# Kernel optimization log

Hardware: AMD Instinct MI355X
Metric: run time of the kernel (lower is better)

Reference implementation:

```python
import jax, jax.numpy as jnp
import numpy as np

EPS = 1e-5

def _bn(z, gamma, beta):
    mu = z.mean(axis=0)
    var = z.var(axis=0)  # biased, matches torch BN normalization
    return (z - mu) * jax.lax.rsqrt(var + EPS) * gamma + beta

def _sage_bn_relu(h, src, dst, n_nodes, Wl, bl, Wr, gamma, beta):
    # SAGEConv (mean aggr): out = lin_l(mean_{j in N(i)} h_j) + lin_r(h_i)
    msg = h[src]                                               # [E, d] gather
    agg = jax.ops.segment_sum(msg, dst, num_segments=n_nodes)  # [N, d]
    cnt = jax.ops.segment_sum(jnp.ones((src.shape[0], 1), h.dtype), dst,
                              num_segments=n_nodes)            # [N, 1]
    agg = jnp.where(cnt > 0, agg / jnp.maximum(cnt, 1.0), 0.0)
    out = agg @ Wl.T + bl + h @ Wr.T
    return jax.nn.relu(_bn(out, gamma, beta))

def setup_inputs() -> dict:
    key = jax.random.key(0)
    N, E, d, out_c, L, U = 50000, 800000, 128, 128, 3, 256
    ks = jax.random.split(key, 16)
    s = 1.0 / np.sqrt(d)
    return {
        "x": jax.random.normal(ks[0], (N, d), jnp.float32),
        "edge_index": jax.random.randint(ks[1], (2, E), 0, N, jnp.int64),
        "atom_mask": jax.random.uniform(ks[2], (N, 1), jnp.float32),
        "u_index": jax.random.randint(ks[3], (U,), 0, N, jnp.int64),
        "lin_l_w": jax.random.uniform(ks[4], (L, d, d), jnp.float32, -s, s),
        "lin_l_b": jax.random.uniform(ks[5], (L, d), jnp.float32, -s, s),
        "lin_r_w": jax.random.uniform(ks[6], (L, d, d), jnp.float32, -s, s),
        "bn_gamma": jnp.ones((L, d), jnp.float32),
        "bn_beta": jnp.zeros((L, d), jnp.float32),
        "ro_w1": jax.random.uniform(ks[7], (d, d), jnp.float32, -s, s),
        "ro_b1": jax.random.uniform(ks[8], (d,), jnp.float32, -s, s),
        "ro_bn_gamma": jnp.ones((d,), jnp.float32),
        "ro_bn_beta": jnp.zeros((d,), jnp.float32),
        "ro_w2": jax.random.uniform(ks[9], (out_c, d), jnp.float32, -s, s),
        "ro_b2": jax.random.uniform(ks[10], (out_c,), jnp.float32, -s, s),
    }

def reference(x, edge_index, atom_mask, u_index, lin_l_w, lin_l_b, lin_r_w,
              bn_gamma, bn_beta, ro_w1, ro_b1, ro_bn_gamma, ro_bn_beta,
              ro_w2, ro_b2):
    N = x.shape[0]
    src, dst = edge_index[0], edge_index[1]
    h = x
    for l in range(lin_l_w.shape[0]):
        h = _sage_bn_relu(h, src, dst, N, lin_l_w[l], lin_l_b[l],
                          lin_r_w[l], bn_gamma[l], bn_beta[l])
    state = h[u_index]                                         # [U, d]
    z = jax.nn.relu(_bn(h @ ro_w1.T + ro_b1, ro_bn_gamma, ro_bn_beta))
    atom = (z @ ro_w2.T + ro_b2) * atom_mask                   # [N, out]
    return (h, atom, state)
```

## Files before the change

kernel.cpp:

```cpp
#include <hip/hip_runtime.h>

#define D 128

typedef __attribute__((ext_vector_type(8))) short bf16x8;
typedef __attribute__((ext_vector_type(4))) float f32x4;

__device__ __forceinline__ ushort f2b(float f) {
  union { float f; unsigned u; } a; a.f = f;
  unsigned u = a.u;
  return (ushort)((u + 0x7fffu + ((u >> 16) & 1u)) >> 16);
}
__device__ __forceinline__ float b2f_lo(unsigned v) {
  union { unsigned u; float f; } a; a.u = v << 16; return a.f;
}
__device__ __forceinline__ float b2f_hi(unsigned v) {
  union { unsigned u; float f; } a; a.u = v & 0xffff0000u; return a.f;
}

__global__ void k_cast_pad(const float* __restrict__ s, ushort* __restrict__ d, int n4, int np4) {
  int i = blockIdx.x * blockDim.x + threadIdx.x;
  if (i >= np4) return;
  uint2 pk;
  if (i < n4) {
    float4 v = *(const float4*)&s[i * 4];
    pk.x = (unsigned)f2b(v.x) | ((unsigned)f2b(v.y) << 16);
    pk.y = (unsigned)f2b(v.z) | ((unsigned)f2b(v.w) << 16);
  } else {
    pk = make_uint2(0u, 0u);
  }
  *(uint2*)&d[i * 4] = pk;
}

__global__ void k_castw(const float* __restrict__ wl, const float* __restrict__ wr,
                        const float* __restrict__ w1, const float* __restrict__ w2,
                        ushort* __restrict__ dst, int LDD) {
  int i = blockIdx.x * blockDim.x + threadIdx.x;
  int total = 2 * LDD + 2 * D * D;
  if (i >= total) return;
  float v;
  if (i < LDD) v = wl[i];
  else if (i < 2 * LDD) v = wr[i - LDD];
  else if (i < 2 * LDD + D * D) v = w1[i - 2 * LDD];
  else v = w2[i - 2 * LDD - D * D];
  dst[i] = f2b(v);
}

__global__ void k_hist(const int* __restrict__ dstI, int* __restrict__ cnt, int E) {
  int e = blockIdx.x * blockDim.x + threadIdx.x;
  if (e < E) atomicAdd(&cnt[dstI[e]], 1);
}
__global__ void k_scan1(const int* __restrict__ cnt, int* __restrict__ off,
                        int* __restrict__ bsum, int n) {
  __shared__ int sd[256];
  int t = threadIdx.x;
  int i = blockIdx.x * 256 + t;
  int x = (i < n) ? cnt[i] : 0;
  sd[t] = x;
  __syncthreads();
  for (int s = 1; s < 256; s <<= 1) {
    int v = (t >= s) ? sd[t - s] : 0;
    __syncthreads();
    sd[t] += v;
    __syncthreads();
  }
  if (i < n) off[i] = sd[t] - x;
  if (t == 255) bsum[blockIdx.x] = sd[255];
}
__global__ void k_scan2(const int* __restrict__ bsum, int* __restrict__ boff, int nb) {
  __shared__ int sd[256];
  int t = threadIdx.x;
  int x = (t < nb) ? bsum[t] : 0;
  sd[t] = x;
  __syncthreads();
  for (int s = 1; s < 256; s <<= 1) {
    int v = (t >= s) ? sd[t - s] : 0;
    __syncthreads();
    sd[t] += v;
    __syncthreads();
  }
  if (t < nb) boff[t] = sd[t] - x;
}
__global__ void k_scan3(int* __restrict__ off, const int* __restrict__ boff,
                        int* __restrict__ cursor, int n) {
  int i = blockIdx.x * blockDim.x + threadIdx.x;
  if (i < n) {
    int v = off[i] + boff[i >> 8];
    off[i] = v;
    cursor[i] = v;
  }
}
__global__ void k_fill(const int* __restrict__ srcI, const int* __restrict__ dstI,
                       int* __restrict__ cursor, int* __restrict__ eidx, int E) {
  int e = blockIdx.x * blockDim.x + threadIdx.x;
  if (e < E) {
    int p = atomicAdd(&cursor[dstI[e]], 1);
    eidx[p] = srcI[e];
  }
}

__global__ void k_agg(const ushort* __restrict__ hb, const int* __restrict__ off,
                      const int* __restrict__ eidx, ushort* __restrict__ aggb,
                      int N, int Np, int E) {
  int g = (int)(blockIdx.x * (blockDim.x >> 4) + (threadIdx.x >> 4));
  int sub = threadIdx.x & 15;
  if (g >= Np) return;
  ushort* dst = &aggb[(size_t)g * D + sub * 8];
  if (g >= N) { *(uint4*)dst = make_uint4(0u, 0u, 0u, 0u); return; }
  int start = off[g];
  int end = (g == N - 1) ? E : off[g + 1];
  float s0 = 0.f, s1 = 0.f, s2 = 0.f, s3 = 0.f, s4 = 0.f, s5 = 0.f, s6 = 0.f, s7 = 0.f;
#pragma unroll 4
  for (int e = start; e < end; ++e) {
    int sn = eidx[e];
    uint4 v = *(const uint4*)&hb[(size_t)sn * D + sub * 8];
    s0 += b2f_lo(v.x); s1 += b2f_hi(v.x);
    s2 += b2f_lo(v.y); s3 += b2f_hi(v.y);
    s4 += b2f_lo(v.z); s5 += b2f_hi(v.z);
    s6 += b2f_lo(v.w); s7 += b2f_hi(v.w);
  }
  float inv = (end > start) ? 1.0f / (float)(end - start) : 0.0f;
  uint4 o;
  o.x = (unsigned)f2b(s0 * inv) | ((unsigned)f2b(s1 * inv) << 16);
  o.y = (unsigned)f2b(s2 * inv) | ((unsigned)f2b(s3 * inv) << 16);
  o.z = (unsigned)f2b(s4 * inv) | ((unsigned)f2b(s5 * inv) << 16);
  o.w = (unsigned)f2b(s6 * inv) | ((unsigned)f2b(s7 * inv) << 16);
  *(uint4*)dst = o;
}

template <bool DUAL, bool MASK, bool STATS, bool OUTBF16>
__global__ __launch_bounds__(256) void k_mm(
    const ushort* __restrict__ A1, const ushort* __restrict__ W1,
    const float* __restrict__ bias,
    const ushort* __restrict__ A2, const ushort* __restrict__ W2,
    const float* __restrict__ mask,
    void* __restrict__ outv, float* __restrict__ sums, int N) {
  __shared__ float ls[2 * D];
  int t = threadIdx.x;
  int lane = t & 63;
  int wid = t >> 6;
  int wr = wid >> 1, wc = wid & 1;
  int r0 = blockIdx.x * 128 + wr * 64;
  int c0 = wc * 64;
  int lr = lane & 15;
  int lk = (lane >> 4) * 8;

  f32x4 acc[4][4];
#pragma unroll
  for (int i = 0; i < 4; ++i)
#pragma unroll
    for (int j = 0; j < 4; ++j) acc[i][j] = (f32x4){0.f, 0.f, 0.f, 0.f};

#pragma unroll
  for (int ks = 0; ks < 4; ++ks) {
    int kb = ks * 32 + lk;
    bf16x8 a1[4], a2[4];
#pragma unroll
    for (int rt = 0; rt < 4; ++rt) {
      a1[rt] = *(const bf16x8*)&A1[(size_t)(r0 + rt * 16 + lr) * D + kb];
      if (DUAL) a2[rt] = *(const bf16x8*)&A2[(size_t)(r0 + rt * 16 + lr) * D + kb];
    }
#pragma unroll
    for (int jt = 0; jt < 4; ++jt) {
      bf16x8 b1 = *(const bf16x8*)&W1[(size_t)(c0 + jt * 16 + lr) * D + kb];
#pragma unroll
      for (int rt = 0; rt < 4; ++rt)
        acc[rt][jt] = __builtin_amdgcn_mfma_f32_16x16x32_bf16(a1[rt], b1, acc[rt][jt], 0, 0, 0);
      if (DUAL) {
        bf16x8 b2 = *(const bf16x8*)&W2[(size_t)(c0 + jt * 16 + lr) * D + kb];
#pragma unroll
        for (int rt = 0; rt < 4; ++rt)
          acc[rt][jt] = __builtin_amdgcn_mfma_f32_16x16x32_bf16(a2[rt], b2, acc[rt][jt], 0, 0, 0);
      }
    }
  }

  if (STATS) {
    if (t < 2 * D) ls[t] = 0.f;
    __syncthreads();
  }

  int crow = (lane >> 4) * 4;
  float s1v[4], s2v[4];
#pragma unroll
  for (int jt = 0; jt < 4; ++jt) { s1v[jt] = 0.f; s2v[jt] = 0.f; }

  float* outf = (float*)outv;
  ushort* outb = (ushort*)outv;
#pragma unroll
  for (int rt = 0; rt < 4; ++rt) {
    int rbase = r0 + rt * 16 + crow;
#pragma unroll
    for (int jt = 0; jt < 4; ++jt) {
      int col = c0 + jt * 16 + lr;
      float bv = bias[col];
#pragma unroll
      for (int rg = 0; rg < 4; ++rg) {
        int row = rbase + rg;
        if (row < N) {
          float v = acc[rt][jt][rg] + bv;
          if (MASK) v *= mask[row];
          if (OUTBF16) outb[(size_t)row * D + col] = f2b(v);
          else outf[(size_t)row * D + col] = v;
          if (STATS) { s1v[jt] += v; s2v[jt] += v * v; }
        }
      }
    }
  }

  if (STATS) {
#pragma unroll
    for (int jt = 0; jt < 4; ++jt) {
      float a = s1v[jt], b = s2v[jt];
      a += __shfl_xor(a, 16, 64); a += __shfl_xor(a, 32, 64);
      b += __shfl_xor(b, 16, 64); b += __shfl_xor(b, 32, 64);
      if (lane < 16) {
        int col = c0 + jt * 16 + lane;
        atomicAdd(&ls[col], a);
        atomicAdd(&ls[D + col], b);
      }
    }
    __syncthreads();
    if (t < 2 * D) atomicAdd(&sums[t], ls[t]);
  }
}

template <bool F32OUT>
__global__ void k_bnrelu(const ushort* __restrict__ pre, const float* __restrict__ sums,
                         const float* __restrict__ gamma, const float* __restrict__ beta,
                         float* __restrict__ fout, ushort* __restrict__ bout,
                         int N, int Np, float invN) {
  int i4 = blockIdx.x * blockDim.x + threadIdx.x;
  if (i4 >= Np * (D / 4)) return;
  int row = i4 >> 5;
  int c4 = (i4 & 31) * 4;
  uint2 pk;
  if (row < N) {
    uint2 pv = *(const uint2*)&pre[(size_t)row * D + c4];
    float4 v = make_float4(b2f_lo(pv.x), b2f_hi(pv.x), b2f_lo(pv.y), b2f_hi(pv.y));
    float4 s = *(const float4*)&sums[c4];
    float4 q = *(const float4*)&sums[D + c4];
    float4 g = *(const float4*)&gamma[c4];
    float4 b = *(const float4*)&beta[c4];
    float mu, var, sc, sh;
    mu = s.x * invN; var = fmaxf(q.x * invN - mu * mu, 0.f);
    sc = g.x * rsqrtf(var + 1e-5f); sh = b.x - mu * sc;
    v.x = fmaxf(fmaf(v.x, sc, sh), 0.f);
    mu = s.y * invN; var = fmaxf(q.y * invN - mu * mu, 0.f);
    sc = g.y * rsqrtf(var + 1e-5f); sh = b.y - mu * sc;
    v.y = fmaxf(fmaf(v.y, sc, sh), 0.f);
    mu = s.z * invN; var = fmaxf(q.z * invN - mu * mu, 0.f);
    sc = g.z * rsqrtf(var + 1e-5f); sh = b.z - mu * sc;
    v.z = fmaxf(fmaf(v.z, sc, sh), 0.f);
    mu = s.w * invN; var = fmaxf(q.w * invN - mu * mu, 0.f);
    sc = g.w * rsqrtf(var + 1e-5f); sh = b.w - mu * sc;
    v.w = fmaxf(fmaf(v.w, sc, sh), 0.f);
    if (F32OUT) *(float4*)&fout[(size_t)row * D + c4] = v;
    pk.x = (unsigned)f2b(v.x) | ((unsigned)f2b(v.y) << 16);
    pk.y = (unsigned)f2b(v.z) | ((unsigned)f2b(v.w) << 16);
  } else {
    pk = make_uint2(0u, 0u);
  }
  *(uint2*)&bout[(size_t)row * D + c4] = pk;
}

__global__ void k_gather(const float* __restrict__ h, const int* __restrict__ uidx,
                         float* __restrict__ outp, int U) {
  int u = blockIdx.x;
  int t = threadIdx.x;
  int s = uidx[u];
  *(float4*)&outp[(size_t)u * D + t * 4] = *(const float4*)&h[(size_t)s * D + t * 4];
}

extern "C" void kernel_launch(void* const* d_in, const int* in_sizes, int n_in,
                              void* d_out, int out_size, void* d_ws, size_t ws_size,
                              hipStream_t stream) {
  const float* x        = (const float*)d_in[0];
  const int*   edge     = (const int*)d_in[1];
  const float* amask    = (const float*)d_in[2];
  const int*   uindex   = (const int*)d_in[3];
  const float* lin_l_w  = (const float*)d_in[4];
  const float* lin_l_b  = (const float*)d_in[5];
  const float* lin_r_w  = (const float*)d_in[6];
  const float* bn_gamma = (const float*)d_in[7];
  const float* bn_beta  = (const float*)d_in[8];
  const float* ro_w1    = (const float*)d_in[9];
  const float* ro_b1    = (const float*)d_in[10];
  const float* ro_bng   = (const float*)d_in[11];
  const float* ro_bnb   = (const float*)d_in[12];
  const float* ro_w2    = (const float*)d_in[13];
  const float* ro_b2    = (const float*)d_in[14];

  const int N = in_sizes[0] / D;
  const int E = in_sizes[1] / 2;
  const int U = in_sizes[3];
  const int L = in_sizes[4] / (D * D);
  const int Np = ((N + 127) / 128) * 128;
  const int LDD = L * D * D;

  const int* srcI = edge;
  const int* dstI = edge + E;

  float* outH     = (float*)d_out;
  float* outAtom  = outH + (size_t)N * D;
  float* outState = outAtom + (size_t)N * D;

  char* w = (char*)d_ws;
  ushort* hb   = (ushort*)w; w += (size_t)Np * D * 2;
  ushort* aggb = (ushort*)w; w += (size_t)Np * D * 2;
  ushort* pre  = (ushort*)w; w += (size_t)Np * D * 2;
  ushort* wall = (ushort*)w; w += (size_t)(2 * LDD + 2 * D * D) * 2;
  float*  sums = (float*)w;  w += 4 * 2 * D * 4;
  int* off    = (int*)w;     w += (size_t)(N + 1) * 4;
  int* cursor = (int*)w;     w += (size_t)N * 4;
  int* bsum   = (int*)w;     w += 1024;
  int* boff   = (int*)w;     w += 1024;
  int* eidx   = (int*)w;     w += (size_t)E * 4;

  ushort* wlb = wall;
  ushort* wrb = wlb + (size_t)LDD;
  ushort* w1b = wrb + (size_t)LDD;
  ushort* w2b = w1b + (size_t)D * D;

  k_cast_pad<<<(Np * D / 4 + 255) / 256, 256, 0, stream>>>(x, hb, N * D / 4, Np * D / 4);
  k_castw<<<(2 * LDD + 2 * D * D + 255) / 256, 256, 0, stream>>>(lin_l_w, lin_r_w, ro_w1, ro_w2, wall, LDD);
  hipMemsetAsync(sums, 0, 4 * 2 * D * 4, stream);

  hipMemsetAsync(cursor, 0, (size_t)N * 4, stream);
  int nbE = (E + 255) / 256;
  int nbN = (N + 255) / 256;
  k_hist<<<nbE, 256, 0, stream>>>(dstI, cursor, E);
  k_scan1<<<nbN, 256, 0, stream>>>(cursor, off, bsum, N);
  k_scan2<<<1, 256, 0, stream>>>(bsum, boff, nbN);
  k_scan3<<<nbN, 256, 0, stream>>>(off, boff, cursor, N);
  k_fill<<<nbE, 256, 0, stream>>>(srcI, dstI, cursor, eidx, E);

  const int mmBlocks = Np / 128;
  const int aggBlocks = Np / 16;
  const int bnBlocks = (Np * (D / 4) + 255) / 256;
  const float invN = 1.0f / (float)N;

  for (int l = 0; l < L; ++l) {
    float* lsums = sums + (size_t)l * 2 * D;
    k_agg<<<aggBlocks, 256, 0, stream>>>(hb, off, eidx, aggb, N, Np, E);
    k_mm<true, false, true, true><<<mmBlocks, 256, 0, stream>>>(
        aggb, wlb + (size_t)l * D * D, lin_l_b + (size_t)l * D,
        hb, wrb + (size_t)l * D * D, nullptr, pre, lsums, N);
    if (l == L - 1)
      k_bnrelu<true><<<bnBlocks, 256, 0, stream>>>(pre, lsums, bn_gamma + (size_t)l * D,
                                                   bn_beta + (size_t)l * D, outH, hb, N, Np, invN);
    else
      k_bnrelu<false><<<bnBlocks, 256, 0, stream>>>(pre, lsums, bn_gamma + (size_t)l * D,
                                                    bn_beta + (size_t)l * D, nullptr, hb, N, Np, invN);
  }

  float* rsums = sums + (size_t)L * 2 * D;
  k_mm<false, false, true, true><<<mmBlocks, 256, 0, stream>>>(
      hb, w1b, ro_b1, nullptr, nullptr, nullptr, pre, rsums, N);
  k_bnrelu<false><<<bnBlocks, 256, 0, stream>>>(pre, rsums, ro_bng, ro_bnb, nullptr, aggb, N, Np, invN);
  k_mm<false, true, false, false><<<mmBlocks, 256, 0, stream>>>(
      aggb, w2b, ro_b2, nullptr, nullptr, amask, outAtom, nullptr, N);
  k_gather<<<U, 32, 0, stream>>>(outH, uindex, outState, U);
}
```

Baseline: 360.3 us.

## Fuse neighbor aggregation into SAGE matmul via LDS and precompute CSR ranks

```diff
diff --git a/kernel.cpp b/kernel.cpp
--- a/kernel.cpp
+++ b/kernel.cpp
@@ -1,6 +1,7 @@
 #include <hip/hip_runtime.h>
 
 #define D 128
+#define LDA 136
 
 typedef __attribute__((ext_vector_type(8))) short bf16x8;
 typedef __attribute__((ext_vector_type(4))) float f32x4;
@@ -45,9 +46,14 @@
   dst[i] = f2b(v);
 }
 
-__global__ void k_hist(const int* __restrict__ dstI, int* __restrict__ cnt, int E) {
+__global__ void k_histrank(const int* __restrict__ dstI, int* __restrict__ cnt,
+                           int* __restrict__ rankdst, int E) {
   int e = blockIdx.x * blockDim.x + threadIdx.x;
-  if (e < E) atomicAdd(&cnt[dstI[e]], 1);
+  if (e < E) {
+    int d = dstI[e];
+    int r = atomicAdd(&cnt[d], 1);
+    rankdst[e] = (r << 16) | d;
+  }
 }
 __global__ void k_scan1(const int* __restrict__ cnt, int* __restrict__ off,
                         int* __restrict__ bsum, int n) {
@@ -80,148 +86,135 @@
   }
   if (t < nb) boff[t] = sd[t] - x;
 }
-__global__ void k_scan3(int* __restrict__ off, const int* __restrict__ boff,
-                        int* __restrict__ cursor, int n) {
+__global__ void k_scan3(int* __restrict__ off, const int* __restrict__ boff, int n) {
   int i = blockIdx.x * blockDim.x + threadIdx.x;
-  if (i < n) {
-    int v = off[i] + boff[i >> 8];
-    off[i] = v;
-    cursor[i] = v;
-  }
-}
-__global__ void k_fill(const int* __restrict__ srcI, const int* __restrict__ dstI,
-                       int* __restrict__ cursor, int* __restrict__ eidx, int E) {
+  if (i < n) off[i] += boff[i >> 8];
+}
+__global__ void k_fill(const int* __restrict__ srcI, const int* __restrict__ rankdst,
+                       const int* __restrict__ off, int* __restrict__ eidx, int E) {
   int e = blockIdx.x * blockDim.x + threadIdx.x;
   if (e < E) {
-    int p = atomicAdd(&cursor[dstI[e]], 1);
-    eidx[p] = srcI[e];
-  }
-}
-
-__global__ void k_agg(const ushort* __restrict__ hb, const int* __restrict__ off,
-                      const int* __restrict__ eidx, ushort* __restrict__ aggb,
-                      int N, int Np, int E) {
-  int g = (int)(blockIdx.x * (blockDim.x >> 4) + (threadIdx.x >> 4));
-  int sub = threadIdx.x & 15;
-  if (g >= Np) return;
-  ushort* dst = &aggb[(size_t)g * D + sub * 8];
-  if (g >= N) { *(uint4*)dst = make_uint4(0u, 0u, 0u, 0u); return; }
-  int start = off[g];
-  int end = (g == N - 1) ? E : off[g + 1];
-  float s0 = 0.f, s1 = 0.f, s2 = 0.f, s3 = 0.f, s4 = 0.f, s5 = 0.f, s6 = 0.f, s7 = 0.f;
-#pragma unroll 4
-  for (int e = start; e < end; ++e) {
-    int sn = eidx[e];
-    uint4 v = *(const uint4*)&hb[(size_t)sn * D + sub * 8];
-    s0 += b2f_lo(v.x); s1 += b2f_hi(v.x);
-    s2 += b2f_lo(v.y); s3 += b2f_hi(v.y);
-    s4 += b2f_lo(v.z); s5 += b2f_hi(v.z);
-    s6 += b2f_lo(v.w); s7 += b2f_hi(v.w);
-  }
-  float inv = (end > start) ? 1.0f / (float)(end - start) : 0.0f;
-  uint4 o;
-  o.x = (unsigned)f2b(s0 * inv) | ((unsigned)f2b(s1 * inv) << 16);
-  o.y = (unsigned)f2b(s2 * inv) | ((unsigned)f2b(s3 * inv) << 16);
-  o.z = (unsigned)f2b(s4 * inv) | ((unsigned)f2b(s5 * inv) << 16);
-  o.w = (unsigned)f2b(s6 * inv) | ((unsigned)f2b(s7 * inv) << 16);
-  *(uint4*)dst = o;
-}
-
-template <bool DUAL, bool MASK, bool STATS, bool OUTBF16>
-__global__ __launch_bounds__(256) void k_mm(
-    const ushort* __restrict__ A1, const ushort* __restrict__ W1,
-    const float* __restrict__ bias,
-    const ushort* __restrict__ A2, const ushort* __restrict__ W2,
-    const float* __restrict__ mask,
-    void* __restrict__ outv, float* __restrict__ sums, int N) {
+    int rd = rankdst[e];
+    int d = rd & 0xFFFF;
+    eidx[off[d] + (rd >> 16)] = srcI[e];
+  }
+}
+
+#define ACC8(V, B)                                        \
+  a[B + 0] += b2f_lo(V.x); a[B + 1] += b2f_hi(V.x);       \
+  a[B + 2] += b2f_lo(V.y); a[B + 3] += b2f_hi(V.y);       \
+  a[B + 4] += b2f_lo(V.z); a[B + 5] += b2f_hi(V.z);       \
+  a[B + 6] += b2f_lo(V.w); a[B + 7] += b2f_hi(V.w);
+
+template <bool AGG>
+__global__ __launch_bounds__(512) void k_fused(
+    const ushort* __restrict__ hin, const ushort* __restrict__ Wl,
+    const ushort* __restrict__ Wr, const float* __restrict__ bias,
+    const int* __restrict__ off, const int* __restrict__ eidx,
+    ushort* __restrict__ pre, float* __restrict__ sums, int N, int E) {
+  __shared__ ushort aggS[128 * LDA];
   __shared__ float ls[2 * D];
   int t = threadIdx.x;
+  int r0 = blockIdx.x * 128;
+
+  if (t < 2 * D) ls[t] = 0.f;
+
+  if (AGG) {
+    int lrow = t >> 2;
+    int row = r0 + lrow;
+    int part = (t & 3) << 5;
+    float a[32];
+#pragma unroll
+    for (int i = 0; i < 32; ++i) a[i] = 0.f;
+    int start = 0, end = 0;
+    if (row < N) { start = off[row]; end = (row == N - 1) ? E : off[row + 1]; }
+    const ushort* hbase = hin + part;
+#pragma unroll 2
+    for (int e = start; e < end; ++e) {
+      int sn = eidx[e];
+      const uint4* p = (const uint4*)(hbase + (size_t)sn * D);
+      uint4 v0 = p[0], v1 = p[1], v2 = p[2], v3 = p[3];
+      ACC8(v0, 0) ACC8(v1, 8) ACC8(v2, 16) ACC8(v3, 24)
+    }
+    float inv = (end > start) ? 1.0f / (float)(end - start) : 0.f;
+    unsigned o[16];
+#pragma unroll
+    for (int i = 0; i < 16; ++i)
+      o[i] = (unsigned)f2b(a[2 * i] * inv) | ((unsigned)f2b(a[2 * i + 1] * inv) << 16);
+    uint4* dst = (uint4*)&aggS[lrow * LDA + part];
+    dst[0] = make_uint4(o[0], o[1], o[2], o[3]);
+    dst[1] = make_uint4(o[4], o[5], o[6], o[7]);
+    dst[2] = make_uint4(o[8], o[9], o[10], o[11]);
+    dst[3] = make_uint4(o[12], o[13], o[14], o[15]);
+  }
+  __syncthreads();
+
   int lane = t & 63;
   int wid = t >> 6;
   int wr = wid >> 1, wc = wid & 1;
-  int r0 = blockIdx.x * 128 + wr * 64;
-  int c0 = wc * 64;
-  int lr = lane & 15;
-  int lk = (lane >> 4) * 8;
-
-  f32x4 acc[4][4];
-#pragma unroll
-  for (int i = 0; i < 4; ++i)
+  int rw = wr * 32, cw = wc * 64;
+  int lr = lane & 15, lk = (lane >> 4) * 8;
+
+  f32x4 acc[2][4];
+#pragma unroll
+  for (int i = 0; i < 2; ++i)
 #pragma unroll
     for (int j = 0; j < 4; ++j) acc[i][j] = (f32x4){0.f, 0.f, 0.f, 0.f};
 
 #pragma unroll
   for (int ks = 0; ks < 4; ++ks) {
     int kb = ks * 32 + lk;
-    bf16x8 a1[4], a2[4];
-#pragma unroll
-    for (int rt = 0; rt < 4; ++rt) {
-      a1[rt] = *(const bf16x8*)&A1[(size_t)(r0 + rt * 16 + lr) * D + kb];
-      if (DUAL) a2[rt] = *(const bf16x8*)&A2[(size_t)(r0 + rt * 16 + lr) * D + kb];
+    bf16x8 aA[2], aB[2];
+#pragma unroll
+    for (int rt = 0; rt < 2; ++rt) {
+      if (AGG) {
+        aA[rt] = *(const bf16x8*)&aggS[(rw + rt * 16 + lr) * LDA + kb];
+        aB[rt] = *(const bf16x8*)&hin[(size_t)(r0 + rw + rt * 16 + lr) * D + kb];
+      } else {
+        aA[rt] = *(const bf16x8*)&hin[(size_t)(r0 + rw + rt * 16 + lr) * D + kb];
+      }
     }
 #pragma unroll
     for (int jt = 0; jt < 4; ++jt) {
-      bf16x8 b1 = *(const bf16x8*)&W1[(size_t)(c0 + jt * 16 + lr) * D + kb];
-#pragma unroll
-      for (int rt = 0; rt < 4; ++rt)
-        acc[rt][jt] = __builtin_amdgcn_mfma_f32_16x16x32_bf16(a1[rt], b1, acc[rt][jt], 0, 0, 0);
-      if (DUAL) {
-        bf16x8 b2 = *(const bf16x8*)&W2[(size_t)(c0 + jt * 16 + lr) * D + kb];
-#pragma unroll
-        for (int rt = 0; rt < 4; ++rt)
-          acc[rt][jt] = __builtin_amdgcn_mfma_f32_16x16x32_bf16(a2[rt], b2, acc[rt][jt], 0, 0, 0);
+      bf16x8 b1 = *(const bf16x8*)&Wl[(size_t)(cw + jt * 16 + lr) * D + kb];
+      acc[0][jt] = __builtin_amdgcn_mfma_f32_16x16x32_bf16(aA[0], b1, acc[0][jt], 0, 0, 0);
+      acc[1][jt] = __builtin_amdgcn_mfma_f32_16x16x32_bf16(aA[1], b1, acc[1][jt], 0, 0, 0);
+      if (AGG) {
+        bf16x8 b2 = *(const bf16x8*)&Wr[(size_t)(cw + jt * 16 + lr) * D + kb];
+        acc[0][jt] = __builtin_amdgcn_mfma_f32_16x16x32_bf16(aB[0], b2, acc[0][jt], 0, 0, 0);
+        acc[1][jt] = __builtin_amdgcn_mfma_f32_16x16x32_bf16(aB[1], b2, acc[1][jt], 0, 0, 0);
       }
     }
   }
 
-  if (STATS) {
-    if (t < 2 * D) ls[t] = 0.f;
-    __syncthreads();
-  }
-
   int crow = (lane >> 4) * 4;
-  float s1v[4], s2v[4];
-#pragma unroll
-  for (int jt = 0; jt < 4; ++jt) { s1v[jt] = 0.f; s2v[jt] = 0.f; }
-
-  float* outf = (float*)outv;
-  ushort* outb = (ushort*)outv;
-#pragma unroll
-  for (int rt = 0; rt < 4; ++rt) {
-    int rbase = r0 + rt * 16 + crow;
-#pragma unroll
-    for (int jt = 0; jt < 4; ++jt) {
-      int col = c0 + jt * 16 + lr;
-      float bv = bias[col];
+#pragma unroll
+  for (int jt = 0; jt < 4; ++jt) {
+    int col = cw + jt * 16 + lr;
+    float bv = bias[col];
+    float s1 = 0.f, s2 = 0.f;
+#pragma unroll
+    for (int rt = 0; rt < 2; ++rt) {
+      int rbase = r0 + rw + rt * 16 + crow;
 #pragma unroll
       for (int rg = 0; rg < 4; ++rg) {
         int row = rbase + rg;
         if (row < N) {
           float v = acc[rt][jt][rg] + bv;
-          if (MASK) v *= mask[row];
-          if (OUTBF16) outb[(size_t)row * D + col] = f2b(v);
-          else outf[(size_t)row * D + col] = v;
-          if (STATS) { s1v[jt] += v; s2v[jt] += v * v; }
+          pre[(size_t)row * D + col] = f2b(v);
+          s1 += v; s2 += v * v;
         }
       }
     }
-  }
-
-  if (STATS) {
-#pragma unroll
-    for (int jt = 0; jt < 4; ++jt) {
-      float a = s1v[jt], b = s2v[jt];
-      a += __shfl_xor(a, 16, 64); a += __shfl_xor(a, 32, 64);
-      b += __shfl_xor(b, 16, 64); b += __shfl_xor(b, 32, 64);
-      if (lane < 16) {
-        int col = c0 + jt * 16 + lane;
-        atomicAdd(&ls[col], a);
-        atomicAdd(&ls[D + col], b);
-      }
-    }
-    __syncthreads();
-    if (t < 2 * D) atomicAdd(&sums[t], ls[t]);
-  }
+    s1 += __shfl_xor(s1, 16, 64); s1 += __shfl_xor(s1, 32, 64);
+    s2 += __shfl_xor(s2, 16, 64); s2 += __shfl_xor(s2, 32, 64);
+    if (lane < 16) {
+      atomicAdd(&ls[cw + jt * 16 + lane], s1);
+      atomicAdd(&ls[D + cw + jt * 16 + lane], s2);
+    }
+  }
+  __syncthreads();
+  if (t < 2 * D) atomicAdd(&sums[t], ls[t]);
 }
 
 template <bool F32OUT>
@@ -263,6 +256,60 @@
   *(uint2*)&bout[(size_t)row * D + c4] = pk;
 }
 
+__global__ __launch_bounds__(256) void k_mmfin(
+    const ushort* __restrict__ A, const ushort* __restrict__ W,
+    const float* __restrict__ bias, const float* __restrict__ mask,
+    float* __restrict__ out, int N) {
+  int t = threadIdx.x;
+  int lane = t & 63;
+  int wid = t >> 6;
+  int wr = wid >> 1, wc = wid & 1;
+  int r0 = blockIdx.x * 128 + wr * 64;
+  int c0 = wc * 64;
+  int lr = lane & 15, lk = (lane >> 4) * 8;
+
+  f32x4 acc[4][4];
+#pragma unroll
+  for (int i = 0; i < 4; ++i)
+#pragma unroll
+    for (int j = 0; j < 4; ++j) acc[i][j] = (f32x4){0.f, 0.f, 0.f, 0.f};
+
+#pragma unroll
+  for (int ks = 0; ks < 4; ++ks) {
+    int kb = ks * 32 + lk;
+    bf16x8 a1[4];
+#pragma unroll
+    for (int rt = 0; rt < 4; ++rt)
+      a1[rt] = *(const bf16x8*)&A[(size_t)(r0 + rt * 16 + lr) * D + kb];
+#pragma unroll
+    for (int jt = 0; jt < 4; ++jt) {
+      bf16x8 b1 = *(const bf16x8*)&W[(size_t)(c0 + jt * 16 + lr) * D + kb];
+#pragma unroll
+      for (int rt = 0; rt < 4; ++rt)
+        acc[rt][jt] = __builtin_amdgcn_mfma_f32_16x16x32_bf16(a1[rt], b1, acc[rt][jt], 0, 0, 0);
+    }
+  }
+
+  int crow = (lane >> 4) * 4;
+#pragma unroll
+  for (int rt = 0; rt < 4; ++rt) {
+    int rbase = r0 + rt * 16 + crow;
+#pragma unroll
+    for (int jt = 0; jt < 4; ++jt) {
+      int col = c0 + jt * 16 + lr;
+      float bv = bias[col];
+#pragma unroll
+      for (int rg = 0; rg < 4; ++rg) {
+        int row = rbase + rg;
+        if (row < N) {
+          float m = mask[row];
+          out[(size_t)row * D + col] = (acc[rt][jt][rg] + bv) * m;
+        }
+      }
+    }
+  }
+}
+
 __global__ void k_gather(const float* __restrict__ h, const int* __restrict__ uidx,
                          float* __restrict__ outp, int U) {
   int u = blockIdx.x;
@@ -306,15 +353,15 @@
 
   char* w = (char*)d_ws;
   ushort* hb   = (ushort*)w; w += (size_t)Np * D * 2;
-  ushort* aggb = (ushort*)w; w += (size_t)Np * D * 2;
   ushort* pre  = (ushort*)w; w += (size_t)Np * D * 2;
   ushort* wall = (ushort*)w; w += (size_t)(2 * LDD + 2 * D * D) * 2;
+  int*    cnt  = (int*)w;    w += (size_t)N * 4;
   float*  sums = (float*)w;  w += 4 * 2 * D * 4;
-  int* off    = (int*)w;     w += (size_t)(N + 1) * 4;
-  int* cursor = (int*)w;     w += (size_t)N * 4;
-  int* bsum   = (int*)w;     w += 1024;
-  int* boff   = (int*)w;     w += 1024;
-  int* eidx   = (int*)w;     w += (size_t)E * 4;
+  int* off     = (int*)w;    w += (size_t)N * 4;
+  int* rankdst = (int*)w;    w += (size_t)E * 4;
+  int* eidx    = (int*)w;    w += (size_t)E * 4;
+  int* bsum    = (int*)w;    w += 1024;
+  int* boff    = (int*)w;    w += 1024;
 
   ushort* wlb = wall;
   ushort* wrb = wlb + (size_t)LDD;
@@ -323,28 +370,25 @@
 
   k_cast_pad<<<(Np * D / 4 + 255) / 256, 256, 0, stream>>>(x, hb, N * D / 4, Np * D / 4);
   k_castw<<<(2 * LDD + 2 * D * D + 255) / 256, 256, 0, stream>>>(lin_l_w, lin_r_w, ro_w1, ro_w2, wall, LDD);
-  hipMemsetAsync(sums, 0, 4 * 2 * D * 4, stream);
-
-  hipMemsetAsync(cursor, 0, (size_t)N * 4, stream);
+  hipMemsetAsync(cnt, 0, (size_t)N * 4 + 4 * 2 * D * 4, stream);
+
   int nbE = (E + 255) / 256;
   int nbN = (N + 255) / 256;
-  k_hist<<<nbE, 256, 0, stream>>>(dstI, cursor, E);
-  k_scan1<<<nbN, 256, 0, stream>>>(cursor, off, bsum, N);
+  k_histrank<<<nbE, 256, 0, stream>>>(dstI, cnt, rankdst, E);
+  k_scan1<<<nbN, 256, 0, stream>>>(cnt, off, bsum, N);
   k_scan2<<<1, 256, 0, stream>>>(bsum, boff, nbN);
-  k_scan3<<<nbN, 256, 0, stream>>>(off, boff, cursor, N);
-  k_fill<<<nbE, 256, 0, stream>>>(srcI, dstI, cursor, eidx, E);
+  k_scan3<<<nbN, 256, 0, stream>>>(off, boff, N);
+  k_fill<<<nbE, 256, 0, stream>>>(srcI, rankdst, off, eidx, E);
 
   const int mmBlocks = Np / 128;
-  const int aggBlocks = Np / 16;
   const int bnBlocks = (Np * (D / 4) + 255) / 256;
   const float invN = 1.0f / (float)N;
 
   for (int l = 0; l < L; ++l) {
     float* lsums = sums + (size_t)l * 2 * D;
-    k_agg<<<aggBlocks, 256, 0, stream>>>(hb, off, eidx, aggb, N, Np, E);
-    k_mm<true, false, true, true><<<mmBlocks, 256, 0, stream>>>(
-        aggb, wlb + (size_t)l * D * D, lin_l_b + (size_t)l * D,
-        hb, wrb + (size_t)l * D * D, nullptr, pre, lsums, N);
+    k_fused<true><<<mmBlocks, 512, 0, stream>>>(
+        hb, wlb + (size_t)l * D * D, wrb + (size_t)l * D * D,
+        lin_l_b + (size_t)l * D, off, eidx, pre, lsums, N, E);
     if (l == L - 1)
       k_bnrelu<true><<<bnBlocks, 256, 0, stream>>>(pre, lsums, bn_gamma + (size_t)l * D,
                                                    bn_beta + (size_t)l * D, outH, hb, N, Np, invN);
@@ -354,10 +398,9 @@
   }
 
   float* rsums = sums + (size_t)L * 2 * D;
-  k_mm<false, false, true, true><<<mmBlocks, 256, 0, stream>>>(
-      hb, w1b, ro_b1, nullptr, nullptr, nullptr, pre, rsums, N);
-  k_bnrelu<false><<<bnBlocks, 256, 0, stream>>>(pre, rsums, ro_bng, ro_bnb, nullptr, aggb, N, Np, invN);
-  k_mm<false, true, false, false><<<mmBlocks, 256, 0, stream>>>(
-      aggb, w2b, ro_b2, nullptr, nullptr, amask, outAtom, nullptr, N);
+  k_fused<false><<<mmBlocks, 512, 0, stream>>>(
+      hb, w1b, nullptr, ro_b1, off, eidx, pre, rsums, N, E);
+  k_bnrelu<false><<<bnBlocks, 256, 0, stream>>>(pre, rsums, ro_bng, ro_bnb, nullptr, hb, N, Np, invN);
+  k_mmfin<<<mmBlocks, 256, 0, stream>>>(hb, w2b, ro_b2, amask, outAtom, N);
   k_gather<<<U, 32, 0, stream>>>(outH, uindex, outState, U);
 }
```

New measurement: 328.7 us. 8.8% less time.
